# Kernel tuning notes

Hardware: AMD Instinct MI355X
Metric: run time of the kernel (lower is better)

Reference implementation:

```python
import jax, jax.numpy as jnp
import numpy as np

L, B, D_IN, D_OUT, K = 2048, 16, 512, 512, 3  # K=3 -> prev=1, after=1 taps for both directions


def setup_inputs() -> dict:
    key = jax.random.key(0)
    ks = jax.random.split(key, 6)
    scale = 1.0 / np.sqrt(D_IN)
    return {
        "input": jax.random.normal(ks[0], (L, B, D_IN), dtype=jnp.float32),
        "lengths": jnp.full((B,), L, dtype=jnp.int32),  # unused by forward body (faithful)
        "fwd_W": jax.random.normal(ks[1], (K, D_IN, 3 * D_OUT), dtype=jnp.float32) * scale,
        "fwd_b": jax.random.normal(ks[2], (K, 3 * D_OUT), dtype=jnp.float32) * scale,
        "rev_W": jax.random.normal(ks[3], (K, D_IN, 3 * D_OUT), dtype=jnp.float32) * scale,
        "rev_b": jax.random.normal(ks[4], (K, 3 * D_OUT), dtype=jnp.float32) * scale,
    }


def _gates(x, W, b):
    # x: [L,B,D_in], W: [K,D_in,3*D_out], b: [K,3*D_out]
    y = jnp.einsum('lbd,kde->klbe', x, W) + b[:, None, None, :]
    out = y[1]  # center tap (previous_size == 1)
    # previous tap: output[1:] += y0[:-1]
    out = out + jnp.concatenate([jnp.zeros_like(y[0][:1]), y[0][:-1]], axis=0)
    # after tap: output[:-1] += y2[1:]
    out = out + jnp.concatenate([y[2][1:], jnp.zeros_like(y[2][:1])], axis=0)
    f, o, z = jnp.split(out, 3, axis=-1)
    return jax.nn.sigmoid(f), jax.nn.sigmoid(o), jnp.tanh(z)


def _pool(f, o, z, init_cell, reverse=False):
    # cell_t = f_t * z_t + (1 - f_t) * cell_{t-1}  (fo-pool linear recurrence)
    def step(c, ft_fzt):
        ft, fzt = ft_fzt
        c = fzt + (1.0 - ft) * c
        return c, c
    _, cells = jax.lax.scan(step, init_cell, (f, f * z), reverse=reverse)
    return cells * o, cells  # lax.scan(reverse=True) stacks in original time order


def reference(input, lengths, fwd_W, fwd_b, rev_W, rev_b):
    init_cell = jnp.zeros((input.shape[1], D_OUT), dtype=input.dtype)
    f, o, z = _gates(input, fwd_W, fwd_b)
    hidden, cell = _pool(f, o, z, init_cell, reverse=False)
    fr, orr, zr = _gates(input, rev_W, rev_b)
    rhidden, rcell = _pool(fr, orr, zr, init_cell, reverse=True)
    output = jnp.concatenate([hidden, rhidden], axis=-1)          # [L,B,2*D_out]
    last_hidden = jnp.concatenate([hidden[-1], rhidden[-1]], -1)  # torch code uses [-1] for both
    last_cell = jnp.concatenate([cell[-1], rcell[-1]], -1)
    return output, last_hidden, last_cell
```

## Files before the change

### kernel.cpp

```cpp
#include <hip/hip_runtime.h>

#define L_SEQ 2048
#define BATCH 16
#define DIN   512
#define NOUT  1536
#define MROWS (L_SEQ*BATCH)
#define PROWS ((L_SEQ+2)*BATCH)
#define NTILES 48

typedef float    f32x4 __attribute__((ext_vector_type(4)));
typedef _Float16 half8 __attribute__((ext_vector_type(8)));

static __device__ __forceinline__ float sigm(float x) { return 1.f / (1.f + __expf(-x)); }
static __device__ __forceinline__ float tanh_f(float x) {
  float ax = fabsf(x);
  float t = __expf(-2.f * ax);
  float r = (1.f - t) / (1.f + t);
  return x < 0.f ? -r : r;
}

__global__ __launch_bounds__(256) void prep_x(const float* __restrict__ x,
                                              _Float16* __restrict__ xh) {
  int gid = blockIdx.x * 256 + threadIdx.x;
  int pr = gid >> 6, seg = gid & 63;
  int l = (pr >> 4) - 1;
  half8 h = (half8)0;
  if (l >= 0 && l < L_SEQ) {
    const float* src = x + (size_t)(pr - 16) * DIN + seg * 8;
#pragma unroll
    for (int i = 0; i < 8; ++i) h[i] = (_Float16)src[i];
  }
  *(half8*)(xh + (size_t)gid * 8) = h;
}

__global__ __launch_bounds__(256) void prep_w(const float* __restrict__ Wf, const float* __restrict__ Wr,
                                              _Float16* __restrict__ wTf, _Float16* __restrict__ wTr) {
  __shared__ float tile[32][33];
  int bid = blockIdx.x;
  int dir = bid & 1; bid >>= 1;
  int et = bid % 48; bid /= 48;
  int dt = bid % 16; int k = bid / 16;
  const float* W = dir ? Wr : Wf;
  _Float16* th = dir ? wTr : wTf;
  int tx = threadIdx.x & 31, ty = threadIdx.x >> 5;
  int d0 = dt * 32, e0 = et * 32;
  const float* Wk = W + (size_t)k * DIN * NOUT;
#pragma unroll
  for (int r = 0; r < 4; ++r)
    tile[ty + r * 8][tx] = Wk[(size_t)(d0 + ty + r * 8) * NOUT + e0 + tx];
  __syncthreads();
#pragma unroll
  for (int r = 0; r < 4; ++r) {
    int e = e0 + ty + r * 8;
    size_t o = (size_t)k * NOUT * DIN + (size_t)e * DIN + d0 + tx;
    th[o] = (_Float16)tile[tx][ty + r * 8];
  }
}

static __device__ __forceinline__ void gload16(const void* g, void* l) {
  __builtin_amdgcn_global_load_lds((const __attribute__((address_space(1))) void*)g,
                                   (__attribute__((address_space(3))) void*)l, 16, 0, 0);
}

__global__ __launch_bounds__(256) void gemm_gates(
    const _Float16* __restrict__ xh,
    const _Float16* __restrict__ wTh,
    const float* __restrict__ bias,
    _Float16* __restrict__ g)
{
  __shared__ _Float16 AB[4 * 4096];
  const int tid = threadIdx.x;
  const int wave = tid >> 6, lane = tid & 63;
  int bid = blockIdx.x;
  const int xcd = bid & 7, t0 = bid >> 3;
  const int mt = xcd * 32 + t0 / 12, nt = t0 % 12;
  const int brow = mt * 128, bcol = nt * 128;

  const int aw_row = lane >> 2;
  const int aw_col = ((lane & 3) ^ ((lane >> 3) & 3)) * 8;

  const _Float16* xbase = xh + (size_t)brow * DIN;
  const _Float16* wbase = wTh + (size_t)bcol * DIN;

  f32x4 acc[4][4];
#pragma unroll
  for (int i = 0; i < 4; ++i)
#pragma unroll
    for (int j = 0; j < 4; ++j) acc[i][j] = (f32x4)(0.f);

  const int wm = (wave >> 1) * 64, wn = (wave & 1) * 64;
  const int fr = lane & 15;
  const int fko = (((lane >> 4) ^ ((fr >> 1) & 3))) * 8;

  auto stage = [&](int t, int buf) {
    int k = t >> 4, kk = (t & 15) * 32;
    const _Float16* xs = xbase + (size_t)(16 * k) * DIN + kk + aw_col;
    const _Float16* ws = wbase + (size_t)k * NOUT * DIN + kk + aw_col;
    _Float16* la = AB + buf * 4096 + (wave * 32) * 32;
    _Float16* lb = AB + 8192 + buf * 4096 + (wave * 32) * 32;
#pragma unroll
    for (int c = 0; c < 2; ++c) {
      size_t roff = (size_t)(wave * 32 + c * 16 + aw_row) * DIN;
      gload16(xs + roff, la + c * 16 * 32);
      gload16(ws + roff, lb + c * 16 * 32);
    }
  };

  stage(0, 0);
  for (int t = 0; t < NTILES; ++t) {
    int buf = t & 1;
    if (t + 1 < NTILES) {
      stage(t + 1, buf ^ 1);
      asm volatile("s_waitcnt vmcnt(4)" ::: "memory");
    } else {
      asm volatile("s_waitcnt vmcnt(0)" ::: "memory");
    }
    __builtin_amdgcn_s_barrier();
    __builtin_amdgcn_sched_barrier(0);
    const _Float16* la = AB + buf * 4096;
    const _Float16* lb = AB + 8192 + buf * 4096;
    half8 a[4], b[4];
#pragma unroll
    for (int i = 0; i < 4; ++i) {
      a[i] = *(const half8*)(la + (wm + i * 16 + fr) * 32 + fko);
      b[i] = *(const half8*)(lb + (wn + i * 16 + fr) * 32 + fko);
    }
#pragma unroll
    for (int i = 0; i < 4; ++i)
#pragma unroll
      for (int j = 0; j < 4; ++j)
        acc[i][j] = __builtin_amdgcn_mfma_f32_16x16x32_f16(a[i], b[j], acc[i][j], 0, 0, 0);
    __builtin_amdgcn_sched_barrier(0);
    __builtin_amdgcn_s_barrier();
  }

  const float* b0 = bias;
  const float* b1 = bias + NOUT;
  const float* b2 = bias + 2 * NOUT;
#pragma unroll
  for (int j = 0; j < 4; ++j) {
    int gcol = bcol + wn + j * 16 + fr;
    float bb0 = b0[gcol], bb1 = b1[gcol], bb2 = b2[gcol];
#pragma unroll
    for (int i = 0; i < 4; ++i) {
#pragma unroll
      for (int q = 0; q < 4; ++q) {
        int grow = brow + wm + i * 16 + (lane >> 4) * 4 + q;
        int l = grow >> 4;
        float bs = bb1 + (l > 0 ? bb0 : 0.f) + (l < L_SEQ - 1 ? bb2 : 0.f);
        g[(size_t)grow * NOUT + gcol] = (_Float16)(acc[i][j][q] + bs);
      }
    }
  }
}

__global__ __launch_bounds__(256) void pool_phase1(const _Float16* __restrict__ g,
                                                   float* __restrict__ Aarr, float* __restrict__ Bvarr,
                                                   int rev) {
  int gid = blockIdx.x * 256 + threadIdx.x;
  int q = gid >> 13, idx = gid & 8191;
  int b = idx >> 9, j = idx & 511;
  const _Float16* gf = g + (size_t)b * NOUT + j;
  float A = 1.f, Bv = 0.f;
  int l0 = q * 64;
#pragma unroll 4
  for (int t = 0; t < 64; ++t) {
    int l = rev ? (l0 + 63 - t) : (l0 + t);
    size_t off = (size_t)l * (BATCH * NOUT);
    float f = sigm((float)gf[off]);
    float z = tanh_f((float)gf[off + 1024]);
    Bv = f * z + (1.f - f) * Bv;
    A *= (1.f - f);
  }
  Aarr[gid] = A;
  Bvarr[gid] = Bv;
}

__global__ __launch_bounds__(256) void pool_phase3(const _Float16* __restrict__ g,
                                                   const float* __restrict__ Aarr,
                                                   const float* __restrict__ Bvarr,
                                                   float* __restrict__ out,
                                                   float* __restrict__ lh, float* __restrict__ lc,
                                                   int rev) {
  int gid = blockIdx.x * 256 + threadIdx.x;
  int q = gid >> 13, idx = gid & 8191;
  int b = idx >> 9, j = idx & 511;
  const _Float16* gf = g + (size_t)b * NOUT + j;
  float c = 0.f;
  if (!rev) {
    for (int s = 0; s < q; ++s) {
      size_t o = (size_t)s * 8192 + idx;
      c = Aarr[o] * c + Bvarr[o];
    }
  } else {
    for (int s = 31; s > q; --s) {
      size_t o = (size_t)s * 8192 + idx;
      c = Aarr[o] * c + Bvarr[o];
    }
  }
  int l0 = q * 64;
#pragma unroll 2
  for (int t = 0; t < 64; ++t) {
    int l = rev ? (l0 + 63 - t) : (l0 + t);
    size_t off = (size_t)l * (BATCH * NOUT);
    float f = sigm((float)gf[off]);
    float o = sigm((float)gf[off + 512]);
    float z = tanh_f((float)gf[off + 1024]);
    c = f * z + (1.f - f) * c;
    float h = c * o;
    out[(size_t)(l * BATCH + b) * 1024 + rev * 512 + j] = h;
    if (l == L_SEQ - 1) {
      lh[b * 1024 + rev * 512 + j] = h;
      lc[b * 1024 + rev * 512 + j] = c;
    }
  }
}

extern "C" void kernel_launch(void* const* d_in, const int* in_sizes, int n_in,
                              void* d_out, int out_size, void* d_ws, size_t ws_size,
                              hipStream_t stream) {
  const float* x    = (const float*)d_in[0];
  const float* fwdW = (const float*)d_in[2];
  const float* fwdb = (const float*)d_in[3];
  const float* revW = (const float*)d_in[4];
  const float* revb = (const float*)d_in[5];

  float* out = (float*)d_out;
  float* lh  = out + (size_t)L_SEQ * BATCH * 1024;
  float* lc  = lh + BATCH * 1024;

  char* ws = (char*)d_ws;
  size_t off = 0;
  _Float16* g = (_Float16*)(ws + off);        off += (size_t)MROWS * NOUT * 2;
  _Float16* xhp = (_Float16*)(ws + off);      off += (size_t)PROWS * DIN * 2;
  _Float16* wTf = (_Float16*)(ws + off);      off += (size_t)3 * NOUT * DIN * 2;
  _Float16* wTr = (_Float16*)(ws + off);      off += (size_t)3 * NOUT * DIN * 2;
  float* Aarr  = (float*)(ws + off); off += (size_t)32 * 8192 * 4;
  float* Bvarr = (float*)(ws + off); off += (size_t)32 * 8192 * 4;

  prep_x<<<8200, 256, 0, stream>>>(x, xhp);
  prep_w<<<4608, 256, 0, stream>>>(fwdW, revW, wTf, wTr);

  for (int dir = 0; dir < 2; ++dir) {
    const _Float16* wh = dir ? wTr : wTf;
    const float* bias = dir ? revb : fwdb;
    gemm_gates<<<3072, 256, 0, stream>>>(xhp, wh, bias, g);
    pool_phase1<<<1024, 256, 0, stream>>>(g, Aarr, Bvarr, dir);
    pool_phase3<<<1024, 256, 0, stream>>>(g, Aarr, Bvarr, out, lh, lc, dir);
  }
}
```

Measured before the change: 553.8 us.

## Merge both directions into single GEMM and pool launches with larger M tiles

Computes forward and reverse gate GEMMs in one launch writing to a gate buffer twice as wide, and runs each pool phase once over both directions. The GEMM tile grows to 256x128 (8x4 MFMA accumulators per wave, more LDS), with launch_bounds occupancy 2 and s_setprio around the MFMA block. This cuts launch count and gives the pool kernels twice the parallelism, at the cost of higher register and LDS pressure per block and a doubled gate workspace.

```diff
diff --git a/kernel.cpp b/kernel.cpp
--- a/kernel.cpp
+++ b/kernel.cpp
@@ -4,6 +4,7 @@
 #define BATCH 16
 #define DIN   512
 #define NOUT  1536
+#define GSTRIDE 3072
 #define MROWS (L_SEQ*BATCH)
 #define PROWS ((L_SEQ+2)*BATCH)
 #define NTILES 48
@@ -62,33 +63,38 @@
                                    (__attribute__((address_space(3))) void*)l, 16, 0, 0);
 }
 
-__global__ __launch_bounds__(256) void gemm_gates(
+__global__ __launch_bounds__(256, 2) void gemm_gates(
     const _Float16* __restrict__ xh,
-    const _Float16* __restrict__ wTh,
-    const float* __restrict__ bias,
+    const _Float16* __restrict__ wTf,
+    const _Float16* __restrict__ wTr,
+    const float* __restrict__ biasf,
+    const float* __restrict__ biasr,
     _Float16* __restrict__ g)
 {
-  __shared__ _Float16 AB[4 * 4096];
+  __shared__ _Float16 AB[24576];
   const int tid = threadIdx.x;
   const int wave = tid >> 6, lane = tid & 63;
   int bid = blockIdx.x;
   const int xcd = bid & 7, t0 = bid >> 3;
-  const int mt = xcd * 32 + t0 / 12, nt = t0 % 12;
-  const int brow = mt * 128, bcol = nt * 128;
-
-  const int aw_row = lane >> 2;
-  const int aw_col = ((lane & 3) ^ ((lane >> 3) & 3)) * 8;
+  const int mt = xcd * 16 + t0 / 24, nt = t0 % 24;
+  const int dir = nt / 12, ntd = nt % 12;
+  const int brow = mt * 256, bcol = ntd * 128;
+
+  const _Float16* wTh = dir ? wTr : wTf;
+  const float* bias   = dir ? biasr : biasf;
+
+  const int aw_col = ((tid & 3) ^ ((tid >> 3) & 3)) * 8;
 
   const _Float16* xbase = xh + (size_t)brow * DIN;
   const _Float16* wbase = wTh + (size_t)bcol * DIN;
 
-  f32x4 acc[4][4];
-#pragma unroll
-  for (int i = 0; i < 4; ++i)
+  f32x4 acc[8][4];
+#pragma unroll
+  for (int i = 0; i < 8; ++i)
 #pragma unroll
     for (int j = 0; j < 4; ++j) acc[i][j] = (f32x4)(0.f);
 
-  const int wm = (wave >> 1) * 64, wn = (wave & 1) * 64;
+  const int wm = (wave >> 1) * 128, wn = (wave & 1) * 64;
   const int fr = lane & 15;
   const int fko = (((lane >> 4) ^ ((fr >> 1) & 3))) * 8;
 
@@ -96,13 +102,15 @@
     int k = t >> 4, kk = (t & 15) * 32;
     const _Float16* xs = xbase + (size_t)(16 * k) * DIN + kk + aw_col;
     const _Float16* ws = wbase + (size_t)k * NOUT * DIN + kk + aw_col;
-    _Float16* la = AB + buf * 4096 + (wave * 32) * 32;
-    _Float16* lb = AB + 8192 + buf * 4096 + (wave * 32) * 32;
+#pragma unroll
+    for (int c = 0; c < 4; ++c) {
+      int row = c * 64 + (tid >> 2);
+      gload16(xs + (size_t)row * DIN, AB + buf * 8192 + (c * 64 + (wave * 16)) * 32);
+    }
 #pragma unroll
     for (int c = 0; c < 2; ++c) {
-      size_t roff = (size_t)(wave * 32 + c * 16 + aw_row) * DIN;
-      gload16(xs + roff, la + c * 16 * 32);
-      gload16(ws + roff, lb + c * 16 * 32);
+      int row = c * 64 + (tid >> 2);
+      gload16(ws + (size_t)row * DIN, AB + 16384 + buf * 4096 + (c * 64 + (wave * 16)) * 32);
     }
   };
 
@@ -111,25 +119,28 @@
     int buf = t & 1;
     if (t + 1 < NTILES) {
       stage(t + 1, buf ^ 1);
-      asm volatile("s_waitcnt vmcnt(4)" ::: "memory");
+      asm volatile("s_waitcnt vmcnt(6)" ::: "memory");
     } else {
       asm volatile("s_waitcnt vmcnt(0)" ::: "memory");
     }
     __builtin_amdgcn_s_barrier();
     __builtin_amdgcn_sched_barrier(0);
-    const _Float16* la = AB + buf * 4096;
-    const _Float16* lb = AB + 8192 + buf * 4096;
-    half8 a[4], b[4];
-#pragma unroll
-    for (int i = 0; i < 4; ++i) {
+    const _Float16* la = AB + buf * 8192;
+    const _Float16* lb = AB + 16384 + buf * 4096;
+    half8 a[8], b[4];
+#pragma unroll
+    for (int i = 0; i < 8; ++i)
       a[i] = *(const half8*)(la + (wm + i * 16 + fr) * 32 + fko);
-      b[i] = *(const half8*)(lb + (wn + i * 16 + fr) * 32 + fko);
-    }
-#pragma unroll
-    for (int i = 0; i < 4; ++i)
+#pragma unroll
+    for (int j = 0; j < 4; ++j)
+      b[j] = *(const half8*)(lb + (wn + j * 16 + fr) * 32 + fko);
+    __builtin_amdgcn_s_setprio(1);
+#pragma unroll
+    for (int i = 0; i < 8; ++i)
 #pragma unroll
       for (int j = 0; j < 4; ++j)
         acc[i][j] = __builtin_amdgcn_mfma_f32_16x16x32_f16(a[i], b[j], acc[i][j], 0, 0, 0);
+    __builtin_amdgcn_s_setprio(0);
     __builtin_amdgcn_sched_barrier(0);
     __builtin_amdgcn_s_barrier();
   }
@@ -139,34 +150,36 @@
   const float* b2 = bias + 2 * NOUT;
 #pragma unroll
   for (int j = 0; j < 4; ++j) {
-    int gcol = bcol + wn + j * 16 + fr;
-    float bb0 = b0[gcol], bb1 = b1[gcol], bb2 = b2[gcol];
-#pragma unroll
-    for (int i = 0; i < 4; ++i) {
+    int col = bcol + wn + j * 16 + fr;
+    float bb0 = b0[col], bb1 = b1[col], bb2 = b2[col];
+    size_t gcol = (size_t)dir * NOUT + col;
+#pragma unroll
+    for (int i = 0; i < 8; ++i) {
 #pragma unroll
       for (int q = 0; q < 4; ++q) {
         int grow = brow + wm + i * 16 + (lane >> 4) * 4 + q;
         int l = grow >> 4;
         float bs = bb1 + (l > 0 ? bb0 : 0.f) + (l < L_SEQ - 1 ? bb2 : 0.f);
-        g[(size_t)grow * NOUT + gcol] = (_Float16)(acc[i][j][q] + bs);
+        g[(size_t)grow * GSTRIDE + gcol] = (_Float16)(acc[i][j][q] + bs);
       }
     }
   }
 }
 
 __global__ __launch_bounds__(256) void pool_phase1(const _Float16* __restrict__ g,
-                                                   float* __restrict__ Aarr, float* __restrict__ Bvarr,
-                                                   int rev) {
+                                                   float* __restrict__ Aarr, float* __restrict__ Bvarr) {
   int gid = blockIdx.x * 256 + threadIdx.x;
-  int q = gid >> 13, idx = gid & 8191;
-  int b = idx >> 9, j = idx & 511;
-  const _Float16* gf = g + (size_t)b * NOUT + j;
+  int rev = gid >> 18;
+  int idx = gid & 262143;
+  int q = idx >> 13, sidx = idx & 8191;
+  int b = sidx >> 9, j = sidx & 511;
+  const _Float16* gf = g + (size_t)b * GSTRIDE + (size_t)rev * NOUT + j;
   float A = 1.f, Bv = 0.f;
   int l0 = q * 64;
 #pragma unroll 4
   for (int t = 0; t < 64; ++t) {
     int l = rev ? (l0 + 63 - t) : (l0 + t);
-    size_t off = (size_t)l * (BATCH * NOUT);
+    size_t off = (size_t)l * (BATCH * GSTRIDE);
     float f = sigm((float)gf[off]);
     float z = tanh_f((float)gf[off + 1024]);
     Bv = f * z + (1.f - f) * Bv;
@@ -180,29 +193,32 @@
                                                    const float* __restrict__ Aarr,
                                                    const float* __restrict__ Bvarr,
                                                    float* __restrict__ out,
-                                                   float* __restrict__ lh, float* __restrict__ lc,
-                                                   int rev) {
+                                                   float* __restrict__ lh, float* __restrict__ lc) {
   int gid = blockIdx.x * 256 + threadIdx.x;
-  int q = gid >> 13, idx = gid & 8191;
-  int b = idx >> 9, j = idx & 511;
-  const _Float16* gf = g + (size_t)b * NOUT + j;
+  int rev = gid >> 18;
+  int idx = gid & 262143;
+  int q = idx >> 13, sidx = idx & 8191;
+  int b = sidx >> 9, j = sidx & 511;
+  const _Float16* gf = g + (size_t)b * GSTRIDE + (size_t)rev * NOUT + j;
+  const float* Ad = Aarr + (size_t)rev * 262144;
+  const float* Bd = Bvarr + (size_t)rev * 262144;
   float c = 0.f;
   if (!rev) {
     for (int s = 0; s < q; ++s) {
-      size_t o = (size_t)s * 8192 + idx;
-      c = Aarr[o] * c + Bvarr[o];
+      size_t o = (size_t)s * 8192 + sidx;
+      c = Ad[o] * c + Bd[o];
     }
   } else {
     for (int s = 31; s > q; --s) {
-      size_t o = (size_t)s * 8192 + idx;
-      c = Aarr[o] * c + Bvarr[o];
+      size_t o = (size_t)s * 8192 + sidx;
+      c = Ad[o] * c + Bd[o];
     }
   }
   int l0 = q * 64;
 #pragma unroll 2
   for (int t = 0; t < 64; ++t) {
     int l = rev ? (l0 + 63 - t) : (l0 + t);
-    size_t off = (size_t)l * (BATCH * NOUT);
+    size_t off = (size_t)l * (BATCH * GSTRIDE);
     float f = sigm((float)gf[off]);
     float o = sigm((float)gf[off + 512]);
     float z = tanh_f((float)gf[off + 1024]);
@@ -231,21 +247,17 @@
 
   char* ws = (char*)d_ws;
   size_t off = 0;
-  _Float16* g = (_Float16*)(ws + off);        off += (size_t)MROWS * NOUT * 2;
+  _Float16* g = (_Float16*)(ws + off);        off += (size_t)MROWS * GSTRIDE * 2;
   _Float16* xhp = (_Float16*)(ws + off);      off += (size_t)PROWS * DIN * 2;
   _Float16* wTf = (_Float16*)(ws + off);      off += (size_t)3 * NOUT * DIN * 2;
   _Float16* wTr = (_Float16*)(ws + off);      off += (size_t)3 * NOUT * DIN * 2;
-  float* Aarr  = (float*)(ws + off); off += (size_t)32 * 8192 * 4;
-  float* Bvarr = (float*)(ws + off); off += (size_t)32 * 8192 * 4;
+  float* Aarr  = (float*)(ws + off); off += (size_t)2 * 32 * 8192 * 4;
+  float* Bvarr = (float*)(ws + off); off += (size_t)2 * 32 * 8192 * 4;
 
   prep_x<<<8200, 256, 0, stream>>>(x, xhp);
   prep_w<<<4608, 256, 0, stream>>>(fwdW, revW, wTf, wTr);
 
-  for (int dir = 0; dir < 2; ++dir) {
-    const _Float16* wh = dir ? wTr : wTf;
-    const float* bias = dir ? revb : fwdb;
-    gemm_gates<<<3072, 256, 0, stream>>>(xhp, wh, bias, g);
-    pool_phase1<<<1024, 256, 0, stream>>>(g, Aarr, Bvarr, dir);
-    pool_phase3<<<1024, 256, 0, stream>>>(g, Aarr, Bvarr, out, lh, lc, dir);
-  }
-}
+  gemm_gates<<<3072, 256, 0, stream>>>(xhp, wTf, wTr, fwdb, revb, g);
+  pool_phase1<<<2048, 256, 0, stream>>>(g, Aarr, Bvarr);
+  pool_phase3<<<2048, 256, 0, stream>>>(g, Aarr, Bvarr, out, lh, lc);
+}
```

New measurement: 463.7 us. -16.3%, faster.
